# Optimization experiments

Hardware: AMD Instinct MI355X
Metric: run time of the kernel (lower is better)

The kernel has to match this reference:

```python
import jax, jax.numpy as jnp
import numpy as np
from jax import lax

LABEL_SIZE = 64
START_ID = 62
PAD_ID = 63
BATCH = 512
SEQ = 512
NEG = -10000.0


def setup_inputs() -> dict:
    key = jax.random.key(0)
    k1, k2, k3, k4 = jax.random.split(key, 4)
    tag_scores = jax.random.normal(k1, (BATCH, SEQ, LABEL_SIZE), dtype=jnp.float32)
    T = 0.1 * jax.random.normal(k2, (LABEL_SIZE, LABEL_SIZE), dtype=jnp.float32)
    # constraints imposed in Model.__init__ on the initial transition matrix
    T = T.at[:, START_ID].set(NEG)
    T = T.at[PAD_ID, :].set(NEG)
    batch_labels = jax.random.randint(k3, (BATCH, SEQ), 0, 62, dtype=jnp.int64)
    lengths = jnp.maximum(jax.random.randint(k4, (BATCH,), 1, SEQ + 1, dtype=jnp.int64), 1)
    return {"tag_scores": tag_scores, "T": T, "batch_labels": batch_labels, "lengths": lengths}


def _crf_loss(tag_scores, T, batch_labels, lengths):
    B, S, L = tag_scores.shape
    mask = jnp.arange(S)[None, :] < lengths[:, None]  # [B,S] contiguous prefix

    # ---- forward algorithm (partition function) ----
    alpha0 = tag_scores[:, 0, :] + T[START_ID, :][None, :]  # [B,L]

    def step(alpha, inp):
        e, m = inp  # e: [B,L] emissions, m: [B] mask
        # scores[b,i,j] = alpha[b,i] + T[i,j] + e[b,j]; reduce over previous label i
        new = jax.nn.logsumexp(alpha[:, :, None] + T[None, :, :] + e[:, None, :], axis=1)
        alpha = jnp.where(m[:, None], new, alpha)
        return alpha, None

    alpha, _ = lax.scan(
        step, alpha0,
        (jnp.swapaxes(tag_scores[:, 1:, :], 0, 1), jnp.swapaxes(mask[:, 1:], 0, 1)),
    )
    final = jax.nn.logsumexp(alpha + T[:, PAD_ID][None, :], axis=1)  # [B]
    forward_scores = final.sum()

    # ---- gold path score ----
    prev = jnp.concatenate(
        [jnp.full((B, 1), START_ID, dtype=batch_labels.dtype), batch_labels[:, :-1]], axis=1
    )  # [B,S]
    trans = T[prev, batch_labels]  # [B,S]
    emit = jnp.take_along_axis(tag_scores, batch_labels[:, :, None], axis=2)[:, :, 0]  # [B,S]
    step_scores = jnp.where(mask, trans + emit, 0.0)
    last_label = jnp.take_along_axis(batch_labels, (lengths - 1)[:, None], axis=1)[:, 0]  # [B]
    gold_scores = step_scores.sum() + T[last_label, PAD_ID].sum()

    return (forward_scores - gold_scores) / B


def reference(tag_scores, T, batch_labels, lengths):
    return _crf_loss(tag_scores, T, batch_labels, lengths)
```

## Files before the change

### kernel.cpp

```cpp
#include <hip/hip_runtime.h>

#define LBL 64
#define SEQN 512
#define BATCHN 512
#define START_ID 62
#define PAD_ID 63
#define CH 8
#define NCH (SEQN / CH)

__global__ __launch_bounds__(64) void crf_batch_kernel(
    const float* __restrict__ ts,
    const float* __restrict__ T,
    const int*   __restrict__ labels,
    const int*   __restrict__ lengths,
    float*       __restrict__ ws)
{
  const int b = blockIdx.x;
  const int j = threadIdx.x;
  const int len = lengths[b];
  const float* __restrict__ e_b = ts + (size_t)b * SEQN * LBL;
  const int* __restrict__ lab_b = labels + b * SEQN;

  float c[LBL];
#pragma unroll
  for (int i = 0; i < LBL; ++i) c[i] = __expf(T[i * LBL + j]);
  const float expPad = __expf(T[j * LBL + PAD_ID]);

  float eC[CH], eN[CH];
#pragma unroll
  for (int r = 0; r < CH; ++r) eC[r] = e_b[r * LBL + j];
#pragma unroll
  for (int r = 0; r < CH; ++r) eN[r] = e_b[(CH + r) * LBL + j];

  float A = __expf(eC[0] + T[START_ID * LBL + j]);
  int E = 0;

  for (int c0 = 0; c0 < NCH; ++c0) {
    const int t0 = c0 * CH;
    if (t0 >= len) break;

#pragma unroll
    for (int tt = 0; tt < CH; ++tt) {
      const int t = t0 + tt;
      if (t >= 1 && t < len) {
        const int Abits = __float_as_int(A);
        unsigned mx = 0u;
        float s0 = 0.f, s1 = 0.f, s2 = 0.f, s3 = 0.f;
#pragma unroll
        for (int k = 0; k < 16; ++k) {
          const float a0 = __int_as_float(__builtin_amdgcn_readlane(Abits, k));
          const float a1 = __int_as_float(__builtin_amdgcn_readlane(Abits, k + 16));
          const float a2 = __int_as_float(__builtin_amdgcn_readlane(Abits, k + 32));
          const float a3 = __int_as_float(__builtin_amdgcn_readlane(Abits, k + 48));
          s0 = fmaf(a0, c[k], s0);
          s1 = fmaf(a1, c[k + 16], s1);
          s2 = fmaf(a2, c[k + 32], s2);
          s3 = fmaf(a3, c[k + 48], s3);
          if ((tt & 3) == 0) {
            unsigned u0 = (unsigned)__float_as_uint(a0);
            unsigned u1 = (unsigned)__float_as_uint(a1);
            unsigned u2 = (unsigned)__float_as_uint(a2);
            unsigned u3 = (unsigned)__float_as_uint(a3);
            unsigned m01 = u0 > u1 ? u0 : u1;
            unsigned m23 = u2 > u3 ? u2 : u3;
            unsigned m = m01 > m23 ? m01 : m23;
            mx = mx > m ? mx : m;
          }
        }
        const float sum = (s0 + s1) + (s2 + s3);
        float ex = __expf(eC[tt]);
        if ((tt & 3) == 0) {
          const int em = (int)(mx >> 23);
          E += 127 - em;
          ex *= __uint_as_float((unsigned)(254 - em) << 23);
        }
        A = sum * ex;
      }
    }

#pragma unroll
    for (int r = 0; r < CH; ++r) eC[r] = eN[r];
    const int tb = (t0 + 2 * CH <= SEQN - CH) ? (t0 + 2 * CH) : (SEQN - CH);
#pragma unroll
    for (int r = 0; r < CH; ++r) eN[r] = e_b[(tb + r) * LBL + j];
  }

  float g = 0.0f;
  for (int t = j; t < len; t += 64) {
    const int l = lab_b[t];
    const int prev = (t == 0) ? START_ID : lab_b[t - 1];
    g += T[prev * LBL + l] + e_b[t * LBL + l];
  }

  float v = A * expPad;
#pragma unroll
  for (int d = 1; d < 64; d <<= 1) {
    v += __shfl_xor(v, d);
    g += __shfl_xor(g, d);
  }

  if (j == 0) {
    const int last = lab_b[len - 1];
    const float gold = g + T[last * LBL + PAD_ID];
    const float fwd = logf(v) - (float)E * 0.69314718055994531f;
    ws[b] = fwd - gold;
  }
}

__global__ __launch_bounds__(256) void crf_reduce_kernel(
    const float* __restrict__ ws, float* __restrict__ out)
{
  __shared__ float red[4];
  const int tid = threadIdx.x;
  float v = ws[tid] + ws[tid + 256];
#pragma unroll
  for (int d = 1; d < 64; d <<= 1) v += __shfl_xor(v, d);
  if ((tid & 63) == 0) red[tid >> 6] = v;
  __syncthreads();
  if (tid == 0) out[0] = (red[0] + red[1] + red[2] + red[3]) * (1.0f / BATCHN);
}

extern "C" void kernel_launch(void* const* d_in, const int* in_sizes, int n_in,
                              void* d_out, int out_size, void* d_ws, size_t ws_size,
                              hipStream_t stream) {
  const float* ts      = (const float*)d_in[0];
  const float* T       = (const float*)d_in[1];
  const int*   labels  = (const int*)d_in[2];
  const int*   lengths = (const int*)d_in[3];
  float* out = (float*)d_out;
  float* ws  = (float*)d_ws;

  crf_batch_kernel<<<BATCHN, 64, 0, stream>>>(ts, T, labels, lengths, ws);
  crf_reduce_kernel<<<1, 256, 0, stream>>>(ws, out);
}
```

Before: 253.7 us.

## Interleave two batch rows per wave with LDS broadcast and packed FMA

Each 64-thread block now runs the forward recurrence for two sequences (b and b+256) in lockstep, interleaving their independent dependency chains to hide latency. The alpha vector is shared through LDS with vector reads instead of readlane broadcasts, and the matrix-vector products use packed 2-wide FMAs over a pairwise-packed transition-exp table. Renormalisation now happens once per 8-step chunk instead of every 4 steps. The cost is half as many blocks (256 on a many-CU GPU), loop length set by the longer of the two sequences, and LDS traffic each step with no barrier.

```diff
diff --git a/kernel.cpp b/kernel.cpp
--- a/kernel.cpp
+++ b/kernel.cpp
@@ -6,7 +6,9 @@
 #define START_ID 62
 #define PAD_ID 63
 #define CH 8
-#define NCH (SEQN / CH)
+
+typedef float v2f __attribute__((ext_vector_type(2)));
+typedef float v4f __attribute__((ext_vector_type(4)));
 
 __global__ __launch_bounds__(64) void crf_batch_kernel(
     const float* __restrict__ ts,
@@ -15,95 +17,159 @@
     const int*   __restrict__ lengths,
     float*       __restrict__ ws)
 {
-  const int b = blockIdx.x;
+  const int b0 = blockIdx.x;
+  const int b1 = b0 + (BATCHN / 2);
   const int j = threadIdx.x;
-  const int len = lengths[b];
-  const float* __restrict__ e_b = ts + (size_t)b * SEQN * LBL;
-  const int* __restrict__ lab_b = labels + b * SEQN;
-
-  float c[LBL];
-#pragma unroll
-  for (int i = 0; i < LBL; ++i) c[i] = __expf(T[i * LBL + j]);
+
+  __shared__ __align__(16) float buf0[LBL];
+  __shared__ __align__(16) float buf1[LBL];
+
+  const int len0 = lengths[b0];
+  const int len1 = lengths[b1];
+  const float* __restrict__ e0 = ts + (size_t)b0 * SEQN * LBL;
+  const float* __restrict__ e1 = ts + (size_t)b1 * SEQN * LBL;
+  const int* __restrict__ lab0 = labels + b0 * SEQN;
+  const int* __restrict__ lab1 = labels + b1 * SEQN;
+
+  v2f c2[32];
+#pragma unroll
+  for (int m = 0; m < 32; ++m) {
+    c2[m].x = __expf(T[(2 * m) * LBL + j]);
+    c2[m].y = __expf(T[(2 * m + 1) * LBL + j]);
+  }
   const float expPad = __expf(T[j * LBL + PAD_ID]);
 
-  float eC[CH], eN[CH];
-#pragma unroll
-  for (int r = 0; r < CH; ++r) eC[r] = e_b[r * LBL + j];
-#pragma unroll
-  for (int r = 0; r < CH; ++r) eN[r] = e_b[(CH + r) * LBL + j];
-
-  float A = __expf(eC[0] + T[START_ID * LBL + j]);
-  int E = 0;
-
-  for (int c0 = 0; c0 < NCH; ++c0) {
-    const int t0 = c0 * CH;
-    if (t0 >= len) break;
-
+  float eC0[CH], eN0[CH], eC1[CH], eN1[CH];
+#pragma unroll
+  for (int r = 0; r < CH; ++r) { eC0[r] = e0[r * LBL + j]; eC1[r] = e1[r * LBL + j]; }
+#pragma unroll
+  for (int r = 0; r < CH; ++r) { eN0[r] = e0[(CH + r) * LBL + j]; eN1[r] = e1[(CH + r) * LBL + j]; }
+
+  float A0 = __expf(eC0[0] + T[START_ID * LBL + j]);
+  float A1 = __expf(eC1[0] + T[START_ID * LBL + j]);
+  int E0 = 0, E1 = 0;
+
+  buf0[j] = A0;
+  buf1[j] = A1;
+
+  const int lenmax = (len0 > len1) ? len0 : len1;
+
+  for (int t0 = 0; t0 < lenmax; t0 += CH) {
 #pragma unroll
     for (int tt = 0; tt < CH; ++tt) {
       const int t = t0 + tt;
-      if (t >= 1 && t < len) {
-        const int Abits = __float_as_int(A);
-        unsigned mx = 0u;
-        float s0 = 0.f, s1 = 0.f, s2 = 0.f, s3 = 0.f;
-#pragma unroll
-        for (int k = 0; k < 16; ++k) {
-          const float a0 = __int_as_float(__builtin_amdgcn_readlane(Abits, k));
-          const float a1 = __int_as_float(__builtin_amdgcn_readlane(Abits, k + 16));
-          const float a2 = __int_as_float(__builtin_amdgcn_readlane(Abits, k + 32));
-          const float a3 = __int_as_float(__builtin_amdgcn_readlane(Abits, k + 48));
-          s0 = fmaf(a0, c[k], s0);
-          s1 = fmaf(a1, c[k + 16], s1);
-          s2 = fmaf(a2, c[k + 32], s2);
-          s3 = fmaf(a3, c[k + 48], s3);
-          if ((tt & 3) == 0) {
-            unsigned u0 = (unsigned)__float_as_uint(a0);
-            unsigned u1 = (unsigned)__float_as_uint(a1);
-            unsigned u2 = (unsigned)__float_as_uint(a2);
-            unsigned u3 = (unsigned)__float_as_uint(a3);
-            unsigned m01 = u0 > u1 ? u0 : u1;
-            unsigned m23 = u2 > u3 ? u2 : u3;
-            unsigned m = m01 > m23 ? m01 : m23;
-            mx = mx > m ? mx : m;
-          }
-        }
-        const float sum = (s0 + s1) + (s2 + s3);
-        float ex = __expf(eC[tt]);
-        if ((tt & 3) == 0) {
-          const int em = (int)(mx >> 23);
-          E += 127 - em;
-          ex *= __uint_as_float((unsigned)(254 - em) << 23);
-        }
-        A = sum * ex;
+      const bool renorm = (tt == 0);
+      const bool act0 = (t >= 1) && (t < len0);
+      const bool act1 = (t >= 1) && (t < len1);
+
+      v2f a00 = {0.f, 0.f}, a01 = {0.f, 0.f}, a02 = {0.f, 0.f}, a03 = {0.f, 0.f};
+      v2f mx0 = {0.f, 0.f};
+#pragma unroll
+      for (int k = 0; k < 16; ++k) {
+        const v4f q = *(const v4f*)(buf0 + 4 * k);
+        const v2f qlo = __builtin_shufflevector(q, q, 0, 1);
+        const v2f qhi = __builtin_shufflevector(q, q, 2, 3);
+        if ((k & 3) == 0) { a00 = __builtin_elementwise_fma(qlo, c2[2 * k], a00);
+                            a01 = __builtin_elementwise_fma(qhi, c2[2 * k + 1], a01); }
+        else if ((k & 3) == 1) { a02 = __builtin_elementwise_fma(qlo, c2[2 * k], a02);
+                            a03 = __builtin_elementwise_fma(qhi, c2[2 * k + 1], a03); }
+        else if ((k & 3) == 2) { a00 = __builtin_elementwise_fma(qlo, c2[2 * k], a00);
+                            a01 = __builtin_elementwise_fma(qhi, c2[2 * k + 1], a01); }
+        else { a02 = __builtin_elementwise_fma(qlo, c2[2 * k], a02);
+               a03 = __builtin_elementwise_fma(qhi, c2[2 * k + 1], a03); }
+        if (renorm) {
+          mx0 = __builtin_elementwise_max(mx0, __builtin_elementwise_max(qlo, qhi));
+        }
+      }
+      {
+        const v2f s2 = (a00 + a01) + (a02 + a03);
+        const float sum = s2.x + s2.y;
+        float ex = __expf(eC0[tt]);
+        int dE = 0;
+        if (renorm) {
+          const float m = fmaxf(mx0.x, mx0.y);
+          const unsigned em = (__float_as_uint(m) >> 23) & 0xffu;
+          ex *= __uint_as_float((254u - em) << 23);
+          dE = 127 - (int)em;
+        }
+        const float nA = sum * ex;
+        A0 = act0 ? nA : A0;
+        if (renorm) E0 += act0 ? dE : 0;
+        buf0[j] = A0;
+      }
+
+      v2f a10 = {0.f, 0.f}, a11 = {0.f, 0.f}, a12 = {0.f, 0.f}, a13 = {0.f, 0.f};
+      v2f mx1 = {0.f, 0.f};
+#pragma unroll
+      for (int k = 0; k < 16; ++k) {
+        const v4f q = *(const v4f*)(buf1 + 4 * k);
+        const v2f qlo = __builtin_shufflevector(q, q, 0, 1);
+        const v2f qhi = __builtin_shufflevector(q, q, 2, 3);
+        if ((k & 3) == 0) { a10 = __builtin_elementwise_fma(qlo, c2[2 * k], a10);
+                            a11 = __builtin_elementwise_fma(qhi, c2[2 * k + 1], a11); }
+        else if ((k & 3) == 1) { a12 = __builtin_elementwise_fma(qlo, c2[2 * k], a12);
+                            a13 = __builtin_elementwise_fma(qhi, c2[2 * k + 1], a13); }
+        else if ((k & 3) == 2) { a10 = __builtin_elementwise_fma(qlo, c2[2 * k], a10);
+                            a11 = __builtin_elementwise_fma(qhi, c2[2 * k + 1], a11); }
+        else { a12 = __builtin_elementwise_fma(qlo, c2[2 * k], a12);
+               a13 = __builtin_elementwise_fma(qhi, c2[2 * k + 1], a13); }
+        if (renorm) {
+          mx1 = __builtin_elementwise_max(mx1, __builtin_elementwise_max(qlo, qhi));
+        }
+      }
+      {
+        const v2f s2 = (a10 + a11) + (a12 + a13);
+        const float sum = s2.x + s2.y;
+        float ex = __expf(eC1[tt]);
+        int dE = 0;
+        if (renorm) {
+          const float m = fmaxf(mx1.x, mx1.y);
+          const unsigned em = (__float_as_uint(m) >> 23) & 0xffu;
+          ex *= __uint_as_float((254u - em) << 23);
+          dE = 127 - (int)em;
+        }
+        const float nA = sum * ex;
+        A1 = act1 ? nA : A1;
+        if (renorm) E1 += act1 ? dE : 0;
+        buf1[j] = A1;
       }
     }
 
 #pragma unroll
-    for (int r = 0; r < CH; ++r) eC[r] = eN[r];
+    for (int r = 0; r < CH; ++r) { eC0[r] = eN0[r]; eC1[r] = eN1[r]; }
     const int tb = (t0 + 2 * CH <= SEQN - CH) ? (t0 + 2 * CH) : (SEQN - CH);
 #pragma unroll
-    for (int r = 0; r < CH; ++r) eN[r] = e_b[(tb + r) * LBL + j];
-  }
-
-  float g = 0.0f;
-  for (int t = j; t < len; t += 64) {
-    const int l = lab_b[t];
-    const int prev = (t == 0) ? START_ID : lab_b[t - 1];
-    g += T[prev * LBL + l] + e_b[t * LBL + l];
-  }
-
-  float v = A * expPad;
+    for (int r = 0; r < CH; ++r) { eN0[r] = e0[(tb + r) * LBL + j]; eN1[r] = e1[(tb + r) * LBL + j]; }
+  }
+
+  float g0 = 0.0f, g1 = 0.0f;
+  for (int t = j; t < len0; t += 64) {
+    const int l = lab0[t];
+    const int prev = (t == 0) ? START_ID : lab0[t - 1];
+    g0 += T[prev * LBL + l] + e0[t * LBL + l];
+  }
+  for (int t = j; t < len1; t += 64) {
+    const int l = lab1[t];
+    const int prev = (t == 0) ? START_ID : lab1[t - 1];
+    g1 += T[prev * LBL + l] + e1[t * LBL + l];
+  }
+
+  float v0 = A0 * expPad;
+  float v1 = A1 * expPad;
 #pragma unroll
   for (int d = 1; d < 64; d <<= 1) {
-    v += __shfl_xor(v, d);
-    g += __shfl_xor(g, d);
+    v0 += __shfl_xor(v0, d);
+    g0 += __shfl_xor(g0, d);
+    v1 += __shfl_xor(v1, d);
+    g1 += __shfl_xor(g1, d);
   }
 
   if (j == 0) {
-    const int last = lab_b[len - 1];
-    const float gold = g + T[last * LBL + PAD_ID];
-    const float fwd = logf(v) - (float)E * 0.69314718055994531f;
-    ws[b] = fwd - gold;
+    const float ln2 = 0.69314718055994531f;
+    const float gold0 = g0 + T[lab0[len0 - 1] * LBL + PAD_ID];
+    const float gold1 = g1 + T[lab1[len1 - 1] * LBL + PAD_ID];
+    ws[b0] = (logf(v0) - (float)E0 * ln2) - gold0;
+    ws[b1] = (logf(v1) - (float)E1 * ln2) - gold1;
   }
 }
 
@@ -130,6 +196,6 @@
   float* out = (float*)d_out;
   float* ws  = (float*)d_ws;
 
-  crf_batch_kernel<<<BATCHN, 64, 0, stream>>>(ts, T, labels, lengths, ws);
+  crf_batch_kernel<<<BATCHN / 2, 64, 0, stream>>>(ts, T, labels, lengths, ws);
   crf_reduce_kernel<<<1, 256, 0, stream>>>(ws, out);
 }
```

Result: slower. 580.2 us (+128.7%).

## Replace readlane broadcast with ds_swizzle/bpermute exchange in CRF forward recurrence

Applied to the files above, without the earlier changes.

Each step of the forward recurrence used to broadcast alpha through 64 scalar readlanes. It now uses one ds_bpermute to swap wave halves and 64 ds_swizzle broadcasts within 32-lane groups, with the transition coefficients split into two 32-entry arrays to match. This moves the broadcast from the scalar path to the LDS-crossbar path and is meant to cut the serial per-step latency. It also precomputes exp of emissions once per chunk, and rescales for the max only once every 8 steps instead of every 4, using a float-max tree. The costs are many LDS-path ops per step, heavy register pressure from bc[64] and m[32], and more exponent headroom needed between rescalings.

```diff
diff --git a/kernel.cpp b/kernel.cpp
--- a/kernel.cpp
+++ b/kernel.cpp
@@ -6,7 +6,6 @@
 #define START_ID 62
 #define PAD_ID 63
 #define CH 8
-#define NCH (SEQN / CH)
 
 __global__ __launch_bounds__(64) void crf_batch_kernel(
     const float* __restrict__ ts,
@@ -21,68 +20,78 @@
   const float* __restrict__ e_b = ts + (size_t)b * SEQN * LBL;
   const int* __restrict__ lab_b = labels + b * SEQN;
 
-  float c[LBL];
+  const int half = j & 32;
+  float c1[32], c2[32];
 #pragma unroll
-  for (int i = 0; i < LBL; ++i) c[i] = __expf(T[i * LBL + j]);
+  for (int k = 0; k < 32; ++k) {
+    c1[k] = __expf(T[(k + half) * LBL + j]);
+    c2[k] = __expf(T[(k + (half ^ 32)) * LBL + j]);
+  }
   const float expPad = __expf(T[j * LBL + PAD_ID]);
+  const int swap_addr = (j ^ 32) << 2;
 
-  float eC[CH], eN[CH];
+  float eC[CH], eNraw[CH];
 #pragma unroll
-  for (int r = 0; r < CH; ++r) eC[r] = e_b[r * LBL + j];
+  for (int r = 0; r < CH; ++r) eC[r] = __expf(e_b[r * LBL + j]);
 #pragma unroll
-  for (int r = 0; r < CH; ++r) eN[r] = e_b[(CH + r) * LBL + j];
+  for (int r = 0; r < CH; ++r) eNraw[r] = e_b[(CH + r) * LBL + j];
 
-  float A = __expf(eC[0] + T[START_ID * LBL + j]);
+  float A = __expf(e_b[j] + T[START_ID * LBL + j]);
   int E = 0;
 
-  for (int c0 = 0; c0 < NCH; ++c0) {
-    const int t0 = c0 * CH;
-    if (t0 >= len) break;
-
+  for (int t0 = 0; t0 < len; t0 += CH) {
 #pragma unroll
     for (int tt = 0; tt < CH; ++tt) {
       const int t = t0 + tt;
       if (t >= 1 && t < len) {
-        const int Abits = __float_as_int(A);
-        unsigned mx = 0u;
-        float s0 = 0.f, s1 = 0.f, s2 = 0.f, s3 = 0.f;
+        const int Ab = __float_as_int(A);
+        const int A2b = __builtin_amdgcn_ds_bpermute(swap_addr, Ab);
+
+        float bc[64];
+#define SWZ_PAIR(K)                                                            \
+        bc[K]      = __int_as_float(__builtin_amdgcn_ds_swizzle(Ab,  (K) << 5)); \
+        bc[32+(K)] = __int_as_float(__builtin_amdgcn_ds_swizzle(A2b, (K) << 5));
+        SWZ_PAIR(0)  SWZ_PAIR(1)  SWZ_PAIR(2)  SWZ_PAIR(3)
+        SWZ_PAIR(4)  SWZ_PAIR(5)  SWZ_PAIR(6)  SWZ_PAIR(7)
+        SWZ_PAIR(8)  SWZ_PAIR(9)  SWZ_PAIR(10) SWZ_PAIR(11)
+        SWZ_PAIR(12) SWZ_PAIR(13) SWZ_PAIR(14) SWZ_PAIR(15)
+        SWZ_PAIR(16) SWZ_PAIR(17) SWZ_PAIR(18) SWZ_PAIR(19)
+        SWZ_PAIR(20) SWZ_PAIR(21) SWZ_PAIR(22) SWZ_PAIR(23)
+        SWZ_PAIR(24) SWZ_PAIR(25) SWZ_PAIR(26) SWZ_PAIR(27)
+        SWZ_PAIR(28) SWZ_PAIR(29) SWZ_PAIR(30) SWZ_PAIR(31)
+#undef SWZ_PAIR
+
+        float s[4] = {0.f, 0.f, 0.f, 0.f};
 #pragma unroll
-        for (int k = 0; k < 16; ++k) {
-          const float a0 = __int_as_float(__builtin_amdgcn_readlane(Abits, k));
-          const float a1 = __int_as_float(__builtin_amdgcn_readlane(Abits, k + 16));
-          const float a2 = __int_as_float(__builtin_amdgcn_readlane(Abits, k + 32));
-          const float a3 = __int_as_float(__builtin_amdgcn_readlane(Abits, k + 48));
-          s0 = fmaf(a0, c[k], s0);
-          s1 = fmaf(a1, c[k + 16], s1);
-          s2 = fmaf(a2, c[k + 32], s2);
-          s3 = fmaf(a3, c[k + 48], s3);
-          if ((tt & 3) == 0) {
-            unsigned u0 = (unsigned)__float_as_uint(a0);
-            unsigned u1 = (unsigned)__float_as_uint(a1);
-            unsigned u2 = (unsigned)__float_as_uint(a2);
-            unsigned u3 = (unsigned)__float_as_uint(a3);
-            unsigned m01 = u0 > u1 ? u0 : u1;
-            unsigned m23 = u2 > u3 ? u2 : u3;
-            unsigned m = m01 > m23 ? m01 : m23;
-            mx = mx > m ? mx : m;
-          }
+        for (int k = 0; k < 32; ++k)
+          s[k & 3] = fmaf(bc[k], c1[k], s[k & 3]);
+#pragma unroll
+        for (int k = 0; k < 32; ++k)
+          s[k & 3] = fmaf(bc[32 + k], c2[k], s[k & 3]);
+
+        float ex = eC[tt];
+        if (tt == 0) {
+          float m[32];
+#pragma unroll
+          for (int k = 0; k < 32; ++k) m[k] = fmaxf(bc[k], bc[32 + k]);
+#pragma unroll
+          for (int st = 16; st >= 1; st >>= 1)
+#pragma unroll
+            for (int k = 0; k < 16; ++k)
+              if (k < st) m[k] = fmaxf(m[k], m[k + st]);
+          const unsigned em = (__float_as_uint(m[0]) >> 23) & 255u;
+          ex *= __uint_as_float((254u - em) << 23);
+          E += 127 - (int)em;
         }
-        const float sum = (s0 + s1) + (s2 + s3);
-        float ex = __expf(eC[tt]);
-        if ((tt & 3) == 0) {
-          const int em = (int)(mx >> 23);
-          E += 127 - em;
-          ex *= __uint_as_float((unsigned)(254 - em) << 23);
-        }
-        A = sum * ex;
+        A = ((s[0] + s[1]) + (s[2] + s[3])) * ex;
       }
     }
 
 #pragma unroll
-    for (int r = 0; r < CH; ++r) eC[r] = eN[r];
+    for (int r = 0; r < CH; ++r) eC[r] = __expf(eNraw[r]);
     const int tb = (t0 + 2 * CH <= SEQN - CH) ? (t0 + 2 * CH) : (SEQN - CH);
 #pragma unroll
-    for (int r = 0; r < CH; ++r) eN[r] = e_b[(tb + r) * LBL + j];
+    for (int r = 0; r < CH; ++r) eNraw[r] = e_b[(tb + r) * LBL + j];
   }
 
   float g = 0.0f;
```

Result: faster. 244.6 us (-3.6%).
